# Kernel tuning notes

Measured on AMD Instinct MI355X. Metric: run time of the kernel, lower is better.

The kernel has to match this reference:

```python
import jax, jax.numpy as jnp
import numpy as np

H = 8          # num heads
D = 16         # head dim
HID = 128      # hidden_dim = H * D
NM, ND, NA = 100000, 20000, 50000
E = 300000     # edges per relation
NUM_CLASSES = 8


def setup_inputs() -> dict:
    key = jax.random.key(0)
    ks = jax.random.split(key, 24)
    s = 0.05
    eye = jnp.eye(D, dtype=jnp.float32)
    inp = {
        'x_movie': jax.random.normal(ks[0], (NM, 256), jnp.float32),
        'x_director': jax.random.normal(ks[1], (ND, 128), jnp.float32),
        'x_actor': jax.random.normal(ks[2], (NA, 128), jnp.float32),
        # edge lists per relation: (director->movie, actor->movie, movie->director, movie->actor)
        'src_dm': jax.random.randint(ks[3], (E,), 0, ND),
        'dst_dm': jax.random.randint(ks[4], (E,), 0, NM),
        'src_am': jax.random.randint(ks[5], (E,), 0, NA),
        'dst_am': jax.random.randint(ks[6], (E,), 0, NM),
        'src_md': jax.random.randint(ks[7], (E,), 0, NM),
        'dst_md': jax.random.randint(ks[8], (E,), 0, ND),
        'src_ma': jax.random.randint(ks[9], (E,), 0, NM),
        'dst_ma': jax.random.randint(ks[10], (E,), 0, NA),
        # per-type pre-encoder (use_pre_encoder=True)
        'Wpre_m': jax.random.normal(ks[11], (256, HID), jnp.float32) * s,
        'Wpre_d': jax.random.normal(ks[12], (128, HID), jnp.float32) * s,
        'Wpre_a': jax.random.normal(ks[13], (128, HID), jnp.float32) * s,
        'bpre': jnp.zeros((3, HID), jnp.float32),
        # per-type K/Q/V projections, stacked over the 3 node types
        'Wk': jax.random.normal(ks[14], (3, HID, HID), jnp.float32) * s,
        'bk': jnp.zeros((3, HID), jnp.float32),
        'Wq': jax.random.normal(ks[15], (3, HID, HID), jnp.float32) * s,
        'bq': jnp.zeros((3, HID), jnp.float32),
        'Wv': jax.random.normal(ks[16], (3, HID, HID), jnp.float32) * s,
        'bv': jnp.zeros((3, HID), jnp.float32),
        # per-relation attention / message matrices and priors (4 relations)
        'a_rel': eye + jax.random.normal(ks[17], (4, H, D, D), jnp.float32) * s,
        'm_rel': eye + jax.random.normal(ks[18], (4, H, D, D), jnp.float32) * s,
        'p_rel': jnp.ones((4, H), jnp.float32),
        # per-type skip gate and output projection
        'skip': jnp.ones((3,), jnp.float32),
        'Wa': jax.random.normal(ks[19], (3, HID, HID), jnp.float32) * s,
        'ba': jnp.zeros((3, HID), jnp.float32),
        # final classification head on target node type ('movie')
        'Wlin': jax.random.normal(ks[20], (HID, NUM_CLASSES), jnp.float32) * s,
        'blin': jnp.zeros((NUM_CLASSES,), jnp.float32),
    }
    return inp


def _seg_softmax_agg(alpha, msg, dst, n):
    # softmax over incoming edges of each destination node, then weighted sum of msgs
    m = jax.ops.segment_max(alpha, dst, num_segments=n)      # [n, H]
    m = jnp.where(jnp.isfinite(m), m, 0.0)
    a = jnp.exp(alpha - m[dst])                              # [E, H]
    denom = jax.ops.segment_sum(a, dst, num_segments=n)      # [n, H]
    num = jax.ops.segment_sum(a[:, :, None] * msg, dst, num_segments=n)  # [n, H, D]
    return num / jnp.maximum(denom, 1e-16)[:, :, None]


def reference(x_movie, x_director, x_actor,
              src_dm, dst_dm, src_am, dst_am, src_md, dst_md, src_ma, dst_ma,
              Wpre_m, Wpre_d, Wpre_a, bpre, Wk, bk, Wq, bq, Wv, bv,
              a_rel, m_rel, p_rel, skip, Wa, ba, Wlin, blin):
    # type order: 0=movie, 1=director, 2=actor
    xs = [x_movie @ Wpre_m + bpre[0],
          x_director @ Wpre_d + bpre[1],
          x_actor @ Wpre_a + bpre[2]]
    k = [(x @ Wk[t] + bk[t]).reshape(-1, H, D) for t, x in enumerate(xs)]
    q = [(x @ Wq[t] + bq[t]).reshape(-1, H, D) for t, x in enumerate(xs)]
    v = [(x @ Wv[t] + bv[t]).reshape(-1, H, D) for t, x in enumerate(xs)]

    # (src_type, dst_type, src_idx, dst_idx) per relation
    rels = [(1, 0, src_dm, dst_dm), (2, 0, src_am, dst_am),
            (0, 1, src_md, dst_md), (0, 2, src_ma, dst_ma)]
    scale = 1.0 / np.sqrt(D).astype(np.float32)
    buckets = {0: [], 1: [], 2: []}
    for r, (st, dt, src, dst) in enumerate(rels):
        ke = jnp.einsum('ehd,hdf->ehf', k[st][src], a_rel[r])          # [E,H,D]
        al = jnp.einsum('ehf,ehf->eh', q[dt][dst], ke) * p_rel[r] * scale
        me = jnp.einsum('ehd,hdf->ehf', v[st][src], m_rel[r])          # [E,H,D]
        buckets[dt].append((al, me, dst))

    n = [x.shape[0] for x in xs]
    outs = []
    for t in range(3):
        al = jnp.concatenate([b[0] for b in buckets[t]], axis=0)
        me = jnp.concatenate([b[1] for b in buckets[t]], axis=0)
        dst = jnp.concatenate([b[2] for b in buckets[t]], axis=0)
        agg = _seg_softmax_agg(al, me, dst, n[t]).reshape(n[t], HID)
        h = jax.nn.gelu(agg, approximate=False) @ Wa[t] + ba[t]
        g = jax.nn.sigmoid(skip[t])
        outs.append(g * h + (1.0 - g) * xs[t])

    return outs[0] @ Wlin + blin
```

## Files before the change

### kernel.cpp

```cpp
#include <hip/hip_runtime.h>
#include <hip/hip_bf16.h>
#include <math.h>

#define NM 100000
#define ND 20000
#define NA 50000
#define EDG 300000
#define CAP 32

typedef __attribute__((ext_vector_type(8))) short shortx8;
typedef __attribute__((ext_vector_type(4))) float floatx4;
typedef __attribute__((ext_vector_type(4))) int intx4;

__device__ __forceinline__ float bf2f(unsigned int u) {
    return __uint_as_float(u << 16);
}
__device__ __forceinline__ unsigned short f2bf(float f) {
    unsigned int x = __float_as_uint(f);
    unsigned int r = x + 0x7fffu + ((x >> 16) & 1u);
    return (unsigned short)(r >> 16);
}
__device__ __forceinline__ unsigned short f2bf_fast(float f) {
    return (unsigned short)((__float_as_uint(f) + 0x8000u) >> 16);
}
__device__ __forceinline__ unsigned int pkbf2(float a, float b) {
    return __builtin_amdgcn_perm(__float_as_uint(b) + 0x8000u,
                                 __float_as_uint(a) + 0x8000u,
                                 0x07060302u);
}
__device__ __forceinline__ float gelu_exact(float x) {
    return 0.5f * x * (1.0f + erff(x * 0.70710678118654752f));
}

static const size_t OFF_BT_Q      = 0;
static const size_t OFF_BT_KAMV_D = 73728;
static const size_t OFF_BT_KAMV_A = 139264;
static const size_t OFF_WKA_D     = 204800;
static const size_t OFF_WVM_D     = 270336;
static const size_t OFF_WKA_A     = 335872;
static const size_t OFF_WVM_A     = 401408;
static const size_t OFF_BQ        = 466944;
static const size_t OFF_B_KAMV_D  = 467520;
static const size_t OFF_B_KAMV_A  = 468544;
static const size_t OFF_BKA_D     = 469568;
static const size_t OFF_BVM_D     = 470080;
static const size_t OFF_BKA_A     = 470592;
static const size_t OFF_BVM_A     = 471104;
static const size_t OFF_WALS      = 471616;
static const size_t OFF_BFIN      = 475712;
static const size_t OFF_Q0        = 524288;
static const size_t OFF_SKIPB     = 26124288;
static const size_t OFF_KAMV_D    = 29324288;
static const size_t OFF_KAMV_A    = 39564288;
static const size_t OFF_COUNTS    = 65164288;
static const size_t OFF_SLOTS     = 65564288;
#define KAMV_A_DELTA 10240000

__global__ __launch_bounds__(256) void precompA(
    const float* __restrict__ Wk, const float* __restrict__ bk,
    const float* __restrict__ Wv, const float* __restrict__ bv,
    const float* __restrict__ Wa, const float* __restrict__ ba,
    const float* __restrict__ Wlin, const float* __restrict__ blin,
    const float* __restrict__ a_rel, const float* __restrict__ m_rel,
    const float* __restrict__ p_rel, const float* __restrict__ skip,
    const float* __restrict__ bpre,
    char* __restrict__ ws)
{
    int tid = blockIdx.x * 256 + threadIdx.x;
    if (tid < 65536) {
        int mat = tid >> 14, rem = tid & 16383;
        int e = rem >> 7, hf = rem & 127, h = hf >> 4, f = hf & 15;
        const float* Wsrc; const float* R; float sc; float* dst;
        if (mat == 0)      { Wsrc = Wk + 16384; R = a_rel;        sc = p_rel[h]     * 0.25f; dst = (float*)(ws + OFF_WKA_D); }
        else if (mat == 1) { Wsrc = Wv + 16384; R = m_rel;        sc = 1.0f;                 dst = (float*)(ws + OFF_WVM_D); }
        else if (mat == 2) { Wsrc = Wk + 32768; R = a_rel + 2048; sc = p_rel[8 + h] * 0.25f; dst = (float*)(ws + OFF_WKA_A); }
        else               { Wsrc = Wv + 32768; R = m_rel + 2048; sc = 1.0f;                 dst = (float*)(ws + OFF_WVM_A); }
        float s = 0.0f;
        for (int d = 0; d < 16; d++)
            s += Wsrc[e * 128 + h * 16 + d] * R[h * 256 + d * 16 + f];
        dst[e * 128 + hf] = s * sc;
    } else if (tid < 66048) {
        int idx = tid - 65536;
        int mat = idx >> 7, hf = idx & 127, h = hf >> 4, f = hf & 15;
        const float* bsrc; const float* R; float sc; float* dst;
        if (mat == 0)      { bsrc = bk + 128; R = a_rel;        sc = p_rel[h]     * 0.25f; dst = (float*)(ws + OFF_BKA_D); }
        else if (mat == 1) { bsrc = bv + 128; R = m_rel;        sc = 1.0f;                 dst = (float*)(ws + OFF_BVM_D); }
        else if (mat == 2) { bsrc = bk + 256; R = a_rel + 2048; sc = p_rel[8 + h] * 0.25f; dst = (float*)(ws + OFF_BKA_A); }
        else               { bsrc = bv + 256; R = m_rel + 2048; sc = 1.0f;                 dst = (float*)(ws + OFF_BVM_A); }
        float s = 0.0f;
        for (int d = 0; d < 16; d++)
            s += bsrc[h * 16 + d] * R[h * 256 + d * 16 + f];
        dst[hf] = s * sc;
    } else if (tid < 67072) {
        int idx = tid - 66048;
        int j = idx >> 3, c = idx & 7;
        float g = 1.0f / (1.0f + __expf(-skip[0]));
        float s = 0.0f;
        for (int o = 0; o < 128; o++)
            s += Wa[j * 128 + o] * Wlin[o * 8 + c];
        ((float*)(ws + OFF_WALS))[j * 8 + c] = g * s;
    } else if (tid < 67080) {
        int c = tid - 67072;
        float g = 1.0f / (1.0f + __expf(-skip[0]));
        float s1 = 0.0f, s2 = 0.0f;
        for (int o = 0; o < 128; o++) {
            s1 += ba[o]   * Wlin[o * 8 + c];
            s2 += bpre[o] * Wlin[o * 8 + c];
        }
        ((float*)(ws + OFF_BFIN))[c] = g * s1 + (1.0f - g) * s2 + blin[c];
    } else if (tid < 67080 + NM) {
        ((int*)(ws + OFF_COUNTS))[tid - 67080] = 0;
    }
}

__global__ __launch_bounds__(256) void precompB(
    const float* __restrict__ Wpre_m, const float* __restrict__ Wpre_d,
    const float* __restrict__ Wpre_a, const float* __restrict__ bpre,
    const float* __restrict__ Wq, const float* __restrict__ bq,
    const float* __restrict__ Wlin, const float* __restrict__ skip,
    char* __restrict__ ws)
{
    int tid = blockIdx.x * 256 + threadIdx.x;
    const float* WKA_D = (const float*)(ws + OFF_WKA_D);
    const float* WVM_D = (const float*)(ws + OFF_WVM_D);
    const float* WKA_A = (const float*)(ws + OFF_WKA_A);
    const float* WVM_A = (const float*)(ws + OFF_WVM_A);

    if (tid < 36864) {
        int n = tid >> 8, c = tid & 255;
        float s = 0.0f;
        if (n < 128) {
            for (int e = 0; e < 128; e++)
                s += Wpre_m[c * 128 + e] * Wq[e * 128 + n];
        } else if (n < 136) {
            int cc = n - 128;
            float g = 1.0f / (1.0f + __expf(-skip[0]));
            for (int e = 0; e < 128; e++)
                s += Wpre_m[c * 128 + e] * Wlin[e * 8 + cc];
            s *= (1.0f - g);
        }
        ((unsigned short*)(ws + OFF_BT_Q))[n * 256 + c] = f2bf(s);
    } else if (tid < 69632) {
        int idx = tid - 36864;
        int nrow = idx >> 7, c = idx & 127;
        const float* Wf = (nrow < 128) ? WKA_D : WVM_D;
        int nc = nrow & 127;
        float s = 0.0f;
        for (int e = 0; e < 128; e++)
            s += Wpre_d[c * 128 + e] * Wf[e * 128 + nc];
        ((unsigned short*)(ws + OFF_BT_KAMV_D))[nrow * 128 + c] = f2bf(s);
    } else if (tid < 102400) {
        int idx = tid - 69632;
        int nrow = idx >> 7, c = idx & 127;
        const float* Wf = (nrow < 128) ? WKA_A : WVM_A;
        int nc = nrow & 127;
        float s = 0.0f;
        for (int e = 0; e < 128; e++)
            s += Wpre_a[c * 128 + e] * Wf[e * 128 + nc];
        ((unsigned short*)(ws + OFF_BT_KAMV_A))[nrow * 128 + c] = f2bf(s);
    } else if (tid < 102544) {
        int n = tid - 102400;
        float s = 0.0f;
        if (n < 128) {
            for (int e = 0; e < 128; e++)
                s += bpre[e] * Wq[e * 128 + n];
            s += bq[n];
        }
        ((float*)(ws + OFF_BQ))[n] = s;
    } else if (tid < 102800) {
        int nrow = tid - 102544;
        const float* Wf  = (nrow < 128) ? WKA_D : WVM_D;
        const float* bf_ = (nrow < 128) ? (const float*)(ws + OFF_BKA_D) : (const float*)(ws + OFF_BVM_D);
        int nc = nrow & 127;
        float s = 0.0f;
        for (int e = 0; e < 128; e++)
            s += bpre[128 + e] * Wf[e * 128 + nc];
        ((float*)(ws + OFF_B_KAMV_D))[nrow] = s + bf_[nc];
    } else if (tid < 103056) {
        int nrow = tid - 102800;
        const float* Wf  = (nrow < 128) ? WKA_A : WVM_A;
        const float* bf_ = (nrow < 128) ? (const float*)(ws + OFF_BKA_A) : (const float*)(ws + OFF_BVM_A);
        int nc = nrow & 127;
        float s = 0.0f;
        for (int e = 0; e < 128; e++)
            s += bpre[256 + e] * Wf[e * 128 + nc];
        ((float*)(ws + OFF_B_KAMV_A))[nrow] = s + bf_[nc];
    }
}

__global__ __launch_bounds__(256) void edge_scatter(
    const int* __restrict__ src_dm, const int* __restrict__ dst_dm,
    const int* __restrict__ src_am, const int* __restrict__ dst_am,
    int* __restrict__ counts, int* __restrict__ slots)
{
    int t = blockIdx.x * 256 + threadIdx.x;
    if (t >= 2 * EDG) return;
    int src, dst, delta;
    if (t < EDG) { src = src_dm[t];       dst = dst_dm[t];       delta = 0; }
    else         { src = src_am[t - EDG]; dst = dst_am[t - EDG]; delta = KAMV_A_DELTA; }
    int pos = atomicAdd(&counts[dst], 1);
    if (pos < CAP) slots[(size_t)dst * CAP + pos] = src * 512 + delta;
}

#define MFMA16(a, b, c) __builtin_amdgcn_mfma_f32_16x16x32_bf16(a, b, c, 0, 0, 0)

template<int NT, bool SKIP>
__global__ __launch_bounds__(256, 2) void gemm_m(
    const float* __restrict__ A, int M,
    const unsigned short* __restrict__ BT,
    const float* __restrict__ bias,
    unsigned short* __restrict__ outb, int ldout,
    float* __restrict__ skipb)
{
    __shared__ unsigned short a_lds[128 * 136];
    __shared__ unsigned short b_lds[NT * 16 * 136];
    int tid = threadIdx.x;
    int w = tid >> 6, lane = tid & 63;
    int quad = lane >> 4, low = lane & 15;
    int rbase = blockIdx.x * 128 + w * 32;

    floatx4 acc[2][NT] = {};

    for (int hfi = 0; hfi < 2; hfi++) {
        if (hfi) __syncthreads();
        for (int idx = tid; idx < NT * 16 * 16; idx += 256) {
            int n = idx >> 4, ch = idx & 15;
            *(intx4*)(&b_lds[n * 136 + ch * 8]) =
                *(const intx4*)(&BT[(size_t)n * 256 + hfi * 128 + ch * 8]);
        }
        for (int f = tid; f < 4096; f += 256) {
            int r = f >> 5, c4 = f & 31;
            int rg = blockIdx.x * 128 + r;
            if (rg >= M) rg = M - 1;
            floatx4 v = *(const floatx4*)(A + (size_t)rg * 256 + hfi * 128 + c4 * 4);
            unsigned long long d =
                ((unsigned long long)pkbf2(v[2], v[3]) << 32) | pkbf2(v[0], v[1]);
            *(unsigned long long*)(&a_lds[r * 136 + c4 * 4]) = d;
        }
        __syncthreads();

        #pragma unroll
        for (int ks = 0; ks < 4; ks++) {
            int ko = ks * 32 + quad * 8;
            shortx8 a0 = *(const shortx8*)(&a_lds[(w * 32 + low) * 136 + ko]);
            shortx8 a1 = *(const shortx8*)(&a_lds[(w * 32 + 16 + low) * 136 + ko]);
            #pragma unroll
            for (int nt = 0; nt < NT; nt++) {
                shortx8 b = *(const shortx8*)(&b_lds[(nt * 16 + low) * 136 + ko]);
                acc[0][nt] = MFMA16(a0, b, acc[0][nt]);
                acc[1][nt] = MFMA16(a1, b, acc[1][nt]);
            }
        }
    }

    #pragma unroll
    for (int mt = 0; mt < 2; mt++) {
        #pragma unroll
        for (int nt = 0; nt < NT; nt++) {
            #pragma unroll
            for (int r = 0; r < 4; r++) {
                int row = rbase + mt * 16 + quad * 4 + r;
                if (row >= M) continue;
                int col = nt * 16 + low;
                float v = acc[mt][nt][r] + bias[col];
                if (SKIP && nt == 8) {
                    if (low < 8) skipb[(size_t)row * 8 + low] = v;
                } else {
                    outb[(size_t)row * ldout + col] = f2bf_fast(v);
                }
            }
        }
    }
}

__global__ __launch_bounds__(256, 2) void gemm_kamv(
    const float* __restrict__ A_d, const float* __restrict__ A_a,
    const unsigned short* __restrict__ BT_d, const unsigned short* __restrict__ BT_a,
    const float* __restrict__ bias_d, const float* __restrict__ bias_a,
    unsigned short* __restrict__ out_d, unsigned short* __restrict__ out_a)
{
    __shared__ unsigned short a_lds[128 * 136];
    __shared__ unsigned short b_lds[128 * 136];
    const int NBLK_D = (ND + 127) / 128;
    bool isD = (int)blockIdx.x < NBLK_D;
    const float* A           = isD ? A_d    : A_a;
    const unsigned short* BT = (isD ? BT_d : BT_a) + (size_t)blockIdx.y * 128 * 128;
    const float* bias        = (isD ? bias_d : bias_a) + blockIdx.y * 128;
    unsigned short* outb     = isD ? out_d  : out_a;
    int M  = isD ? ND : NA;
    int bx = isD ? (int)blockIdx.x : (int)blockIdx.x - NBLK_D;
    int col_off = blockIdx.y * 128;

    int tid = threadIdx.x;
    int w = tid >> 6, lane = tid & 63;
    int quad = lane >> 4, low = lane & 15;
    int rbase = bx * 128 + w * 32;

    for (int idx = tid; idx < 2048; idx += 256) {
        int n = idx >> 4, ch = idx & 15;
        *(intx4*)(&b_lds[n * 136 + ch * 8]) =
            *(const intx4*)(&BT[(size_t)n * 128 + ch * 8]);
    }
    for (int f = tid; f < 4096; f += 256) {
        int r = f >> 5, c4 = f & 31;
        int rg = bx * 128 + r;
        if (rg >= M) rg = M - 1;
        floatx4 v = *(const floatx4*)(A + (size_t)rg * 128 + c4 * 4);
        unsigned long long d =
            ((unsigned long long)pkbf2(v[2], v[3]) << 32) | pkbf2(v[0], v[1]);
        *(unsigned long long*)(&a_lds[r * 136 + c4 * 4]) = d;
    }
    __syncthreads();

    floatx4 acc[2][8] = {};
    #pragma unroll
    for (int ks = 0; ks < 4; ks++) {
        int ko = ks * 32 + quad * 8;
        shortx8 a0 = *(const shortx8*)(&a_lds[(w * 32 + low) * 136 + ko]);
        shortx8 a1 = *(const shortx8*)(&a_lds[(w * 32 + 16 + low) * 136 + ko]);
        #pragma unroll
        for (int nt = 0; nt < 8; nt++) {
            shortx8 b = *(const shortx8*)(&b_lds[(nt * 16 + low) * 136 + ko]);
            acc[0][nt] = MFMA16(a0, b, acc[0][nt]);
            acc[1][nt] = MFMA16(a1, b, acc[1][nt]);
        }
    }

    #pragma unroll
    for (int mt = 0; mt < 2; mt++) {
        #pragma unroll
        for (int nt = 0; nt < 8; nt++) {
            #pragma unroll
            for (int r = 0; r < 4; r++) {
                int row = rbase + mt * 16 + quad * 4 + r;
                if (row >= M) continue;
                int col = nt * 16 + low;
                outb[(size_t)row * 256 + col_off + col] = f2bf_fast(acc[mt][nt][r] + bias[col]);
            }
        }
    }
}

__global__ __launch_bounds__(256) void agg_kernel(
    const unsigned short* __restrict__ q0,
    const char* __restrict__ kamv0,
    const int* __restrict__ counts, const int* __restrict__ slots,
    const float* __restrict__ skipb,
    const float* __restrict__ WaLs, const float* __restrict__ bfin,
    float* __restrict__ out)
{
    __shared__ float wals[1032];
    for (int i = threadIdx.x; i < 1024; i += 256) {
        int c = i >> 7, rem = i & 127, j = rem >> 4, L = rem & 15;
        wals[i] = WaLs[(L * 8 + j) * 8 + c];
    }
    if (threadIdx.x < 8) wals[1024 + threadIdx.x] = bfin[threadIdx.x];
    __syncthreads();

    int lane = threadIdx.x & 63;
    int grp = lane >> 4;
    int L   = lane & 15;
    int n = blockIdx.x * 16 + (threadIdx.x >> 6) * 4 + grp;

    intx4 qv = *(const intx4*)(q0 + (size_t)n * 128 + L * 8);
    float qf[8];
    #pragma unroll
    for (int d = 0; d < 4; d++) {
        unsigned int u = (unsigned int)qv[d];
        qf[2 * d]     = __uint_as_float(u << 16);
        qf[2 * d + 1] = __uint_as_float(u & 0xffff0000u);
    }

    int cnt = counts[n];
    cnt = cnt < 0 ? 0 : (cnt > CAP ? CAP : cnt);
    int s0 = slots[(size_t)n * CAP + L];

    float acc[8] = {0, 0, 0, 0, 0, 0, 0, 0};
    float den = 0.0f;
    for (int i = 0; i < cnt; i++) {
        int off = __shfl(s0, (lane & 48) + (i & 15));
        if (__builtin_expect(i >= 16, 0)) off = slots[(size_t)n * CAP + i];
        const char* p = kamv0 + off;
        intx4 ku = *(const intx4*)(p + L * 16);
        intx4 mu = *(const intx4*)(p + 256 + L * 16);
        float ph = 0.0f;
        #pragma unroll
        for (int d = 0; d < 4; d++) {
            unsigned int u = (unsigned int)ku[d];
            ph += qf[2 * d]     * __uint_as_float(u << 16);
            ph += qf[2 * d + 1] * __uint_as_float(u & 0xffff0000u);
        }
        float pf = ph + __shfl_xor(ph, 1);
        float wgt = __expf(fminf(pf, 60.0f));
        den += wgt;
        #pragma unroll
        for (int d = 0; d < 4; d++) {
            unsigned int u = (unsigned int)mu[d];
            acc[2 * d]     += wgt * __uint_as_float(u << 16);
            acc[2 * d + 1] += wgt * __uint_as_float(u & 0xffff0000u);
        }
    }
    float inv = 1.0f / fmaxf(den, 1e-16f);

    float part[8] = {0, 0, 0, 0, 0, 0, 0, 0};
    #pragma unroll
    for (int j = 0; j < 8; j++) {
        float u = gelu_exact(acc[j] * inv);
        #pragma unroll
        for (int c = 0; c < 8; c++)
            part[c] += u * wals[c * 128 + j * 16 + L];
    }

    bool b0 = lane & 1, b1 = lane & 2, b2 = lane & 4;
    float t1[4], t2[2], t3;
    #pragma unroll
    for (int k = 0; k < 4; k++) {
        float send = b0 ? part[k] : part[4 + k];
        float got  = __shfl_xor(send, 1);
        t1[k] = (b0 ? part[4 + k] : part[k]) + got;
    }
    #pragma unroll
    for (int k = 0; k < 2; k++) {
        float send = b1 ? t1[k] : t1[2 + k];
        float got  = __shfl_xor(send, 2);
        t2[k] = (b1 ? t1[2 + k] : t1[k]) + got;
    }
    {
        float send = b2 ? t2[0] : t2[1];
        float got  = __shfl_xor(send, 4);
        t3 = (b2 ? t2[1] : t2[0]) + got;
    }
    t3 += __shfl_xor(t3, 8);
    if (L < 8) {
        int c = 4 * (L & 1) + 2 * ((L >> 1) & 1) + ((L >> 2) & 1);
        out[(size_t)n * 8 + c] = t3 + skipb[(size_t)n * 8 + c] + wals[1024 + c];
    }
}

extern "C" void kernel_launch(void* const* d_in, const int* in_sizes, int n_in,
                              void* d_out, int out_size, void* d_ws, size_t ws_size,
                              hipStream_t stream) {
    (void)in_sizes; (void)n_in; (void)out_size; (void)ws_size;
    const float* x_movie    = (const float*)d_in[0];
    const float* x_director = (const float*)d_in[1];
    const float* x_actor    = (const float*)d_in[2];
    const int* src_dm = (const int*)d_in[3];
    const int* dst_dm = (const int*)d_in[4];
    const int* src_am = (const int*)d_in[5];
    const int* dst_am = (const int*)d_in[6];
    const float* Wpre_m = (const float*)d_in[11];
    const float* Wpre_d = (const float*)d_in[12];
    const float* Wpre_a = (const float*)d_in[13];
    const float* bpre   = (const float*)d_in[14];
    const float* Wk     = (const float*)d_in[15];
    const float* bk     = (const float*)d_in[16];
    const float* Wq     = (const float*)d_in[17];
    const float* bq     = (const float*)d_in[18];
    const float* Wv     = (const float*)d_in[19];
    const float* bv     = (const float*)d_in[20];
    const float* a_rel  = (const float*)d_in[21];
    const float* m_rel  = (const float*)d_in[22];
    const float* p_rel  = (const float*)d_in[23];
    const float* skip   = (const float*)d_in[24];
    const float* Wa     = (const float*)d_in[25];
    const float* ba     = (const float*)d_in[26];
    const float* Wlin   = (const float*)d_in[27];
    const float* blin   = (const float*)d_in[28];

    char* ws = (char*)d_ws;
    float* out = (float*)d_out;

    precompA<<<(67080 + NM + 255) / 256, 256, 0, stream>>>(
        Wk, bk, Wv, bv, Wa, ba, Wlin, blin,
        a_rel, m_rel, p_rel, skip, bpre, ws);
    precompB<<<403, 256, 0, stream>>>(Wpre_m, Wpre_d, Wpre_a, bpre,
                                      Wq, bq, Wlin, skip, ws);

    edge_scatter<<<(2 * EDG + 255) / 256, 256, 0, stream>>>(
        src_dm, dst_dm, src_am, dst_am,
        (int*)(ws + OFF_COUNTS), (int*)(ws + OFF_SLOTS));

    gemm_m<9, true><<<(NM + 127) / 128, 256, 0, stream>>>(
        x_movie, NM, (const unsigned short*)(ws + OFF_BT_Q),
        (const float*)(ws + OFF_BQ),
        (unsigned short*)(ws + OFF_Q0), 128, (float*)(ws + OFF_SKIPB));

    gemm_kamv<<<dim3((ND + 127) / 128 + (NA + 127) / 128, 2), 256, 0, stream>>>(
        x_director, x_actor,
        (const unsigned short*)(ws + OFF_BT_KAMV_D),
        (const unsigned short*)(ws + OFF_BT_KAMV_A),
        (const float*)(ws + OFF_B_KAMV_D), (const float*)(ws + OFF_B_KAMV_A),
        (unsigned short*)(ws + OFF_KAMV_D), (unsigned short*)(ws + OFF_KAMV_A));

    agg_kernel<<<NM / 16, 256, 0, stream>>>(
        (const unsigned short*)(ws + OFF_Q0),
        (const char*)(ws + OFF_KAMV_D),
        (const int*)(ws + OFF_COUNTS), (const int*)(ws + OFF_SLOTS),
        (const float*)(ws + OFF_SKIPB),
        (const float*)(ws + OFF_WALS), (const float*)(ws + OFF_BFIN), out);
}
```

Measured before the change: 446.9 us.

## Merge precompute, edge scatter and GEMM launches; transpose weights for vectorized dot products

The precompB and edge_scatter kernels are folded into one launch, and the movie and director/actor GEMMs into a single gemm_all launch with block-range dispatch. This cuts launch count and the idle tails between dependent small kernels. Wq and the fused K/V weights are stored transposed so the precompute dot products read contiguous memory with float4 loads instead of strided loops. The GEMM loads are restructured to fetch global data into registers before writing to LDS. WQT reuses the SKIPB workspace offset, which is only safe because the transposed Wq is consumed before gemm_all writes skipb.

```diff
diff --git a/kernel.cpp b/kernel.cpp
--- a/kernel.cpp
+++ b/kernel.cpp
@@ -7,6 +7,7 @@
 #define NA 50000
 #define EDG 300000
 #define CAP 32
+#define NBLK_M 782
 
 typedef __attribute__((ext_vector_type(8))) short shortx8;
 typedef __attribute__((ext_vector_type(4))) float floatx4;
@@ -50,6 +51,7 @@
 static const size_t OFF_BFIN      = 475712;
 static const size_t OFF_Q0        = 524288;
 static const size_t OFF_SKIPB     = 26124288;
+static const size_t OFF_WQT       = 26124288;
 static const size_t OFF_KAMV_D    = 29324288;
 static const size_t OFF_KAMV_A    = 39564288;
 static const size_t OFF_COUNTS    = 65164288;
@@ -63,7 +65,7 @@
     const float* __restrict__ Wlin, const float* __restrict__ blin,
     const float* __restrict__ a_rel, const float* __restrict__ m_rel,
     const float* __restrict__ p_rel, const float* __restrict__ skip,
-    const float* __restrict__ bpre,
+    const float* __restrict__ bpre, const float* __restrict__ Wq,
     char* __restrict__ ws)
 {
     int tid = blockIdx.x * 256 + threadIdx.x;
@@ -78,7 +80,7 @@
         float s = 0.0f;
         for (int d = 0; d < 16; d++)
             s += Wsrc[e * 128 + h * 16 + d] * R[h * 256 + d * 16 + f];
-        dst[e * 128 + hf] = s * sc;
+        dst[hf * 128 + e] = s * sc;
     } else if (tid < 66048) {
         int idx = tid - 65536;
         int mat = idx >> 7, hf = idx & 127, h = hf >> 4, f = hf & 15;
@@ -108,30 +110,61 @@
             s2 += bpre[o] * Wlin[o * 8 + c];
         }
         ((float*)(ws + OFF_BFIN))[c] = g * s1 + (1.0f - g) * s2 + blin[c];
-    } else if (tid < 67080 + NM) {
-        ((int*)(ws + OFF_COUNTS))[tid - 67080] = 0;
-    }
-}
-
-__global__ __launch_bounds__(256) void precompB(
+    } else if (tid < 83464) {
+        int i = tid - 67080;
+        int n = i >> 7, e = i & 127;
+        ((float*)(ws + OFF_WQT))[n * 128 + e] = Wq[e * 128 + n];
+    } else if (tid < 83464 + NM) {
+        ((int*)(ws + OFF_COUNTS))[tid - 83464] = 0;
+    }
+}
+
+__device__ __forceinline__ float dot128(const float* __restrict__ a,
+                                        const float* __restrict__ b) {
+    const floatx4* x = (const floatx4*)a;
+    const floatx4* y = (const floatx4*)b;
+    float s = 0.0f;
+    #pragma unroll
+    for (int i = 0; i < 32; i++) {
+        floatx4 u = x[i], v = y[i];
+        s += u[0] * v[0] + u[1] * v[1] + u[2] * v[2] + u[3] * v[3];
+    }
+    return s;
+}
+
+__global__ __launch_bounds__(256) void prep_scat(
+    const int* __restrict__ src_dm, const int* __restrict__ dst_dm,
+    const int* __restrict__ src_am, const int* __restrict__ dst_am,
     const float* __restrict__ Wpre_m, const float* __restrict__ Wpre_d,
     const float* __restrict__ Wpre_a, const float* __restrict__ bpre,
-    const float* __restrict__ Wq, const float* __restrict__ bq,
-    const float* __restrict__ Wlin, const float* __restrict__ skip,
+    const float* __restrict__ bq, const float* __restrict__ Wlin,
+    const float* __restrict__ skip,
     char* __restrict__ ws)
 {
-    int tid = blockIdx.x * 256 + threadIdx.x;
+    if (blockIdx.x < 2344) {
+        int t = blockIdx.x * 256 + threadIdx.x;
+        if (t >= 2 * EDG) return;
+        int src, dst, delta;
+        if (t < EDG) { src = src_dm[t];       dst = dst_dm[t];       delta = 0; }
+        else         { src = src_am[t - EDG]; dst = dst_am[t - EDG]; delta = KAMV_A_DELTA; }
+        int* counts = (int*)(ws + OFF_COUNTS);
+        int* slots  = (int*)(ws + OFF_SLOTS);
+        int pos = atomicAdd(&counts[dst], 1);
+        if (pos < CAP) slots[(size_t)dst * CAP + pos] = src * 512 + delta;
+        return;
+    }
+    int tid = (blockIdx.x - 2344) * 256 + threadIdx.x;
     const float* WKA_D = (const float*)(ws + OFF_WKA_D);
     const float* WVM_D = (const float*)(ws + OFF_WVM_D);
     const float* WKA_A = (const float*)(ws + OFF_WKA_A);
     const float* WVM_A = (const float*)(ws + OFF_WVM_A);
+    const float* WqT   = (const float*)(ws + OFF_WQT);
 
     if (tid < 36864) {
         int n = tid >> 8, c = tid & 255;
         float s = 0.0f;
         if (n < 128) {
-            for (int e = 0; e < 128; e++)
-                s += Wpre_m[c * 128 + e] * Wq[e * 128 + n];
+            s = dot128(Wpre_m + c * 128, WqT + n * 128);
         } else if (n < 136) {
             int cc = n - 128;
             float g = 1.0f / (1.0f + __expf(-skip[0]));
@@ -143,199 +176,184 @@
     } else if (tid < 69632) {
         int idx = tid - 36864;
         int nrow = idx >> 7, c = idx & 127;
-        const float* Wf = (nrow < 128) ? WKA_D : WVM_D;
+        const float* WfT = (nrow < 128) ? WKA_D : WVM_D;
         int nc = nrow & 127;
-        float s = 0.0f;
-        for (int e = 0; e < 128; e++)
-            s += Wpre_d[c * 128 + e] * Wf[e * 128 + nc];
+        float s = dot128(Wpre_d + c * 128, WfT + nc * 128);
         ((unsigned short*)(ws + OFF_BT_KAMV_D))[nrow * 128 + c] = f2bf(s);
     } else if (tid < 102400) {
         int idx = tid - 69632;
         int nrow = idx >> 7, c = idx & 127;
-        const float* Wf = (nrow < 128) ? WKA_A : WVM_A;
+        const float* WfT = (nrow < 128) ? WKA_A : WVM_A;
         int nc = nrow & 127;
-        float s = 0.0f;
-        for (int e = 0; e < 128; e++)
-            s += Wpre_a[c * 128 + e] * Wf[e * 128 + nc];
+        float s = dot128(Wpre_a + c * 128, WfT + nc * 128);
         ((unsigned short*)(ws + OFF_BT_KAMV_A))[nrow * 128 + c] = f2bf(s);
     } else if (tid < 102544) {
         int n = tid - 102400;
         float s = 0.0f;
-        if (n < 128) {
-            for (int e = 0; e < 128; e++)
-                s += bpre[e] * Wq[e * 128 + n];
-            s += bq[n];
-        }
+        if (n < 128) s = dot128(bpre, WqT + n * 128) + bq[n];
         ((float*)(ws + OFF_BQ))[n] = s;
     } else if (tid < 102800) {
         int nrow = tid - 102544;
-        const float* Wf  = (nrow < 128) ? WKA_D : WVM_D;
+        const float* WfT = (nrow < 128) ? WKA_D : WVM_D;
         const float* bf_ = (nrow < 128) ? (const float*)(ws + OFF_BKA_D) : (const float*)(ws + OFF_BVM_D);
         int nc = nrow & 127;
-        float s = 0.0f;
-        for (int e = 0; e < 128; e++)
-            s += bpre[128 + e] * Wf[e * 128 + nc];
-        ((float*)(ws + OFF_B_KAMV_D))[nrow] = s + bf_[nc];
+        ((float*)(ws + OFF_B_KAMV_D))[nrow] = dot128(bpre + 128, WfT + nc * 128) + bf_[nc];
     } else if (tid < 103056) {
         int nrow = tid - 102800;
-        const float* Wf  = (nrow < 128) ? WKA_A : WVM_A;
+        const float* WfT = (nrow < 128) ? WKA_A : WVM_A;
         const float* bf_ = (nrow < 128) ? (const float*)(ws + OFF_BKA_A) : (const float*)(ws + OFF_BVM_A);
         int nc = nrow & 127;
-        float s = 0.0f;
-        for (int e = 0; e < 128; e++)
-            s += bpre[256 + e] * Wf[e * 128 + nc];
-        ((float*)(ws + OFF_B_KAMV_A))[nrow] = s + bf_[nc];
-    }
-}
-
-__global__ __launch_bounds__(256) void edge_scatter(
-    const int* __restrict__ src_dm, const int* __restrict__ dst_dm,
-    const int* __restrict__ src_am, const int* __restrict__ dst_am,
-    int* __restrict__ counts, int* __restrict__ slots)
-{
-    int t = blockIdx.x * 256 + threadIdx.x;
-    if (t >= 2 * EDG) return;
-    int src, dst, delta;
-    if (t < EDG) { src = src_dm[t];       dst = dst_dm[t];       delta = 0; }
-    else         { src = src_am[t - EDG]; dst = dst_am[t - EDG]; delta = KAMV_A_DELTA; }
-    int pos = atomicAdd(&counts[dst], 1);
-    if (pos < CAP) slots[(size_t)dst * CAP + pos] = src * 512 + delta;
+        ((float*)(ws + OFF_B_KAMV_A))[nrow] = dot128(bpre + 256, WfT + nc * 128) + bf_[nc];
+    }
 }
 
 #define MFMA16(a, b, c) __builtin_amdgcn_mfma_f32_16x16x32_bf16(a, b, c, 0, 0, 0)
 
-template<int NT, bool SKIP>
-__global__ __launch_bounds__(256, 2) void gemm_m(
-    const float* __restrict__ A, int M,
-    const unsigned short* __restrict__ BT,
-    const float* __restrict__ bias,
-    unsigned short* __restrict__ outb, int ldout,
-    float* __restrict__ skipb)
+__global__ __launch_bounds__(256, 2) void gemm_all(
+    const float* __restrict__ xm, const float* __restrict__ xd,
+    const float* __restrict__ xa,
+    const unsigned short* __restrict__ btq,
+    const unsigned short* __restrict__ btd,
+    const unsigned short* __restrict__ bta,
+    const float* __restrict__ bq,
+    const float* __restrict__ bbd, const float* __restrict__ bba,
+    unsigned short* __restrict__ q0, float* __restrict__ skipb,
+    unsigned short* __restrict__ outd, unsigned short* __restrict__ outa)
 {
     __shared__ unsigned short a_lds[128 * 136];
-    __shared__ unsigned short b_lds[NT * 16 * 136];
+    __shared__ unsigned short b_lds[144 * 136];
     int tid = threadIdx.x;
     int w = tid >> 6, lane = tid & 63;
     int quad = lane >> 4, low = lane & 15;
-    int rbase = blockIdx.x * 128 + w * 32;
-
-    floatx4 acc[2][NT] = {};
-
-    for (int hfi = 0; hfi < 2; hfi++) {
-        if (hfi) __syncthreads();
-        for (int idx = tid; idx < NT * 16 * 16; idx += 256) {
-            int n = idx >> 4, ch = idx & 15;
-            *(intx4*)(&b_lds[n * 136 + ch * 8]) =
-                *(const intx4*)(&BT[(size_t)n * 256 + hfi * 128 + ch * 8]);
-        }
-        for (int f = tid; f < 4096; f += 256) {
-            int r = f >> 5, c4 = f & 31;
-            int rg = blockIdx.x * 128 + r;
-            if (rg >= M) rg = M - 1;
-            floatx4 v = *(const floatx4*)(A + (size_t)rg * 256 + hfi * 128 + c4 * 4);
+    int bx = blockIdx.x;
+
+    if (bx < NBLK_M) {
+        int row0 = bx * 128;
+        floatx4 acc[2][9] = {};
+        for (int hfi = 0; hfi < 2; hfi++) {
+            if (hfi) __syncthreads();
+            intx4 bvv[9];
+            #pragma unroll
+            for (int it = 0; it < 9; it++) {
+                int idx = it * 256 + tid, n = idx >> 4, ch = idx & 15;
+                bvv[it] = *(const intx4*)&btq[(size_t)n * 256 + hfi * 128 + ch * 8];
+            }
+            floatx4 av[16];
+            #pragma unroll
+            for (int it = 0; it < 16; it++) {
+                int f = it * 256 + tid, r = f >> 5, c4 = f & 31;
+                int rg = row0 + r; if (rg >= NM) rg = NM - 1;
+                av[it] = *(const floatx4*)(xm + (size_t)rg * 256 + hfi * 128 + c4 * 4);
+            }
+            #pragma unroll
+            for (int it = 0; it < 9; it++) {
+                int idx = it * 256 + tid, n = idx >> 4, ch = idx & 15;
+                *(intx4*)&b_lds[n * 136 + ch * 8] = bvv[it];
+            }
+            #pragma unroll
+            for (int it = 0; it < 16; it++) {
+                int f = it * 256 + tid, r = f >> 5, c4 = f & 31;
+                unsigned long long d =
+                    ((unsigned long long)pkbf2(av[it][2], av[it][3]) << 32) |
+                    pkbf2(av[it][0], av[it][1]);
+                *(unsigned long long*)&a_lds[r * 136 + c4 * 4] = d;
+            }
+            __syncthreads();
+            #pragma unroll
+            for (int ks = 0; ks < 4; ks++) {
+                int ko = ks * 32 + quad * 8;
+                shortx8 a0 = *(const shortx8*)&a_lds[(w * 32 + low) * 136 + ko];
+                shortx8 a1 = *(const shortx8*)&a_lds[(w * 32 + 16 + low) * 136 + ko];
+                #pragma unroll
+                for (int nt = 0; nt < 9; nt++) {
+                    shortx8 b = *(const shortx8*)&b_lds[(nt * 16 + low) * 136 + ko];
+                    acc[0][nt] = MFMA16(a0, b, acc[0][nt]);
+                    acc[1][nt] = MFMA16(a1, b, acc[1][nt]);
+                }
+            }
+        }
+        int rb = row0 + w * 32;
+        #pragma unroll
+        for (int mt = 0; mt < 2; mt++) {
+            #pragma unroll
+            for (int nt = 0; nt < 9; nt++) {
+                #pragma unroll
+                for (int r = 0; r < 4; r++) {
+                    int row = rb + mt * 16 + quad * 4 + r;
+                    if (row >= NM) continue;
+                    int col = nt * 16 + low;
+                    float v = acc[mt][nt][r] + bq[col];
+                    if (nt == 8) {
+                        if (low < 8) skipb[(size_t)row * 8 + low] = v;
+                    } else {
+                        q0[(size_t)row * 128 + col] = f2bf_fast(v);
+                    }
+                }
+            }
+        }
+    } else {
+        int rem = bx - NBLK_M;
+        const float* A; const unsigned short* BT; const float* bias;
+        unsigned short* outb; int M, kbx, cofs;
+        if (rem < 157)      { A = xd; BT = btd;             bias = bbd;       outb = outd; M = ND; kbx = rem;       cofs = 0;   }
+        else if (rem < 314) { A = xd; BT = btd + 128 * 128; bias = bbd + 128; outb = outd; M = ND; kbx = rem - 157; cofs = 128; }
+        else if (rem < 705) { A = xa; BT = bta;             bias = bba;       outb = outa; M = NA; kbx = rem - 314; cofs = 0;   }
+        else                { A = xa; BT = bta + 128 * 128; bias = bba + 128; outb = outa; M = NA; kbx = rem - 705; cofs = 128; }
+        int row0 = kbx * 128;
+
+        intx4 bvv[8];
+        #pragma unroll
+        for (int it = 0; it < 8; it++) {
+            int idx = it * 256 + tid, n = idx >> 4, ch = idx & 15;
+            bvv[it] = *(const intx4*)&BT[(size_t)n * 128 + ch * 8];
+        }
+        floatx4 av[16];
+        #pragma unroll
+        for (int it = 0; it < 16; it++) {
+            int f = it * 256 + tid, r = f >> 5, c4 = f & 31;
+            int rg = row0 + r; if (rg >= M) rg = M - 1;
+            av[it] = *(const floatx4*)(A + (size_t)rg * 128 + c4 * 4);
+        }
+        #pragma unroll
+        for (int it = 0; it < 8; it++) {
+            int idx = it * 256 + tid, n = idx >> 4, ch = idx & 15;
+            *(intx4*)&b_lds[n * 136 + ch * 8] = bvv[it];
+        }
+        #pragma unroll
+        for (int it = 0; it < 16; it++) {
+            int f = it * 256 + tid, r = f >> 5, c4 = f & 31;
             unsigned long long d =
-                ((unsigned long long)pkbf2(v[2], v[3]) << 32) | pkbf2(v[0], v[1]);
-            *(unsigned long long*)(&a_lds[r * 136 + c4 * 4]) = d;
+                ((unsigned long long)pkbf2(av[it][2], av[it][3]) << 32) |
+                pkbf2(av[it][0], av[it][1]);
+            *(unsigned long long*)&a_lds[r * 136 + c4 * 4] = d;
         }
         __syncthreads();
 
+        floatx4 acc[2][8] = {};
         #pragma unroll
         for (int ks = 0; ks < 4; ks++) {
             int ko = ks * 32 + quad * 8;
-            shortx8 a0 = *(const shortx8*)(&a_lds[(w * 32 + low) * 136 + ko]);
-            shortx8 a1 = *(const shortx8*)(&a_lds[(w * 32 + 16 + low) * 136 + ko]);
-            #pragma unroll
-            for (int nt = 0; nt < NT; nt++) {
-                shortx8 b = *(const shortx8*)(&b_lds[(nt * 16 + low) * 136 + ko]);
+            shortx8 a0 = *(const shortx8*)&a_lds[(w * 32 + low) * 136 + ko];
+            shortx8 a1 = *(const shortx8*)&a_lds[(w * 32 + 16 + low) * 136 + ko];
+            #pragma unroll
+            for (int nt = 0; nt < 8; nt++) {
+                shortx8 b = *(const shortx8*)&b_lds[(nt * 16 + low) * 136 + ko];
                 acc[0][nt] = MFMA16(a0, b, acc[0][nt]);
                 acc[1][nt] = MFMA16(a1, b, acc[1][nt]);
             }
         }
-    }
-
-    #pragma unroll
-    for (int mt = 0; mt < 2; mt++) {
-        #pragma unroll
-        for (int nt = 0; nt < NT; nt++) {
-            #pragma unroll
-            for (int r = 0; r < 4; r++) {
-                int row = rbase + mt * 16 + quad * 4 + r;
-                if (row >= M) continue;
-                int col = nt * 16 + low;
-                float v = acc[mt][nt][r] + bias[col];
-                if (SKIP && nt == 8) {
-                    if (low < 8) skipb[(size_t)row * 8 + low] = v;
-                } else {
-                    outb[(size_t)row * ldout + col] = f2bf_fast(v);
+        int rb = row0 + w * 32;
+        #pragma unroll
+        for (int mt = 0; mt < 2; mt++) {
+            #pragma unroll
+            for (int nt = 0; nt < 8; nt++) {
+                #pragma unroll
+                for (int r = 0; r < 4; r++) {
+                    int row = rb + mt * 16 + quad * 4 + r;
+                    if (row >= M) continue;
+                    int col = nt * 16 + low;
+                    outb[(size_t)row * 256 + cofs + col] = f2bf_fast(acc[mt][nt][r] + bias[col]);
                 }
-            }
-        }
-    }
-}
-
-__global__ __launch_bounds__(256, 2) void gemm_kamv(
-    const float* __restrict__ A_d, const float* __restrict__ A_a,
-    const unsigned short* __restrict__ BT_d, const unsigned short* __restrict__ BT_a,
-    const float* __restrict__ bias_d, const float* __restrict__ bias_a,
-    unsigned short* __restrict__ out_d, unsigned short* __restrict__ out_a)
-{
-    __shared__ unsigned short a_lds[128 * 136];
-    __shared__ unsigned short b_lds[128 * 136];
-    const int NBLK_D = (ND + 127) / 128;
-    bool isD = (int)blockIdx.x < NBLK_D;
-    const float* A           = isD ? A_d    : A_a;
-    const unsigned short* BT = (isD ? BT_d : BT_a) + (size_t)blockIdx.y * 128 * 128;
-    const float* bias        = (isD ? bias_d : bias_a) + blockIdx.y * 128;
-    unsigned short* outb     = isD ? out_d  : out_a;
-    int M  = isD ? ND : NA;
-    int bx = isD ? (int)blockIdx.x : (int)blockIdx.x - NBLK_D;
-    int col_off = blockIdx.y * 128;
-
-    int tid = threadIdx.x;
-    int w = tid >> 6, lane = tid & 63;
-    int quad = lane >> 4, low = lane & 15;
-    int rbase = bx * 128 + w * 32;
-
-    for (int idx = tid; idx < 2048; idx += 256) {
-        int n = idx >> 4, ch = idx & 15;
-        *(intx4*)(&b_lds[n * 136 + ch * 8]) =
-            *(const intx4*)(&BT[(size_t)n * 128 + ch * 8]);
-    }
-    for (int f = tid; f < 4096; f += 256) {
-        int r = f >> 5, c4 = f & 31;
-        int rg = bx * 128 + r;
-        if (rg >= M) rg = M - 1;
-        floatx4 v = *(const floatx4*)(A + (size_t)rg * 128 + c4 * 4);
-        unsigned long long d =
-            ((unsigned long long)pkbf2(v[2], v[3]) << 32) | pkbf2(v[0], v[1]);
-        *(unsigned long long*)(&a_lds[r * 136 + c4 * 4]) = d;
-    }
-    __syncthreads();
-
-    floatx4 acc[2][8] = {};
-    #pragma unroll
-    for (int ks = 0; ks < 4; ks++) {
-        int ko = ks * 32 + quad * 8;
-        shortx8 a0 = *(const shortx8*)(&a_lds[(w * 32 + low) * 136 + ko]);
-        shortx8 a1 = *(const shortx8*)(&a_lds[(w * 32 + 16 + low) * 136 + ko]);
-        #pragma unroll
-        for (int nt = 0; nt < 8; nt++) {
-            shortx8 b = *(const shortx8*)(&b_lds[(nt * 16 + low) * 136 + ko]);
-            acc[0][nt] = MFMA16(a0, b, acc[0][nt]);
-            acc[1][nt] = MFMA16(a1, b, acc[1][nt]);
-        }
-    }
-
-    #pragma unroll
-    for (int mt = 0; mt < 2; mt++) {
-        #pragma unroll
-        for (int nt = 0; nt < 8; nt++) {
-            #pragma unroll
-            for (int r = 0; r < 4; r++) {
-                int row = rbase + mt * 16 + quad * 4 + r;
-                if (row >= M) continue;
-                int col = nt * 16 + low;
-                outb[(size_t)row * 256 + col_off + col] = f2bf_fast(acc[mt][nt][r] + bias[col]);
             }
         }
     }
@@ -470,26 +488,22 @@
     char* ws = (char*)d_ws;
     float* out = (float*)d_out;
 
-    precompA<<<(67080 + NM + 255) / 256, 256, 0, stream>>>(
+    precompA<<<(83464 + NM + 255) / 256, 256, 0, stream>>>(
         Wk, bk, Wv, bv, Wa, ba, Wlin, blin,
-        a_rel, m_rel, p_rel, skip, bpre, ws);
-    precompB<<<403, 256, 0, stream>>>(Wpre_m, Wpre_d, Wpre_a, bpre,
-                                      Wq, bq, Wlin, skip, ws);
-
-    edge_scatter<<<(2 * EDG + 255) / 256, 256, 0, stream>>>(
+        a_rel, m_rel, p_rel, skip, bpre, Wq, ws);
+
+    prep_scat<<<2344 + 403, 256, 0, stream>>>(
         src_dm, dst_dm, src_am, dst_am,
-        (int*)(ws + OFF_COUNTS), (int*)(ws + OFF_SLOTS));
-
-    gemm_m<9, true><<<(NM + 127) / 128, 256, 0, stream>>>(
-        x_movie, NM, (const unsigned short*)(ws + OFF_BT_Q),
-        (const float*)(ws + OFF_BQ),
-        (unsigned short*)(ws + OFF_Q0), 128, (float*)(ws + OFF_SKIPB));
-
-    gemm_kamv<<<dim3((ND + 127) / 128 + (NA + 127) / 128, 2), 256, 0, stream>>>(
-        x_director, x_actor,
+        Wpre_m, Wpre_d, Wpre_a, bpre, bq, Wlin, skip, ws);
+
+    gemm_all<<<NBLK_M + 1096, 256, 0, stream>>>(
+        x_movie, x_director, x_actor,
+        (const unsigned short*)(ws + OFF_BT_Q),
         (const unsigned short*)(ws + OFF_BT_KAMV_D),
         (const unsigned short*)(ws + OFF_BT_KAMV_A),
+        (const float*)(ws + OFF_BQ),
         (const float*)(ws + OFF_B_KAMV_D), (const float*)(ws + OFF_B_KAMV_A),
+        (unsigned short*)(ws + OFF_Q0), (float*)(ws + OFF_SKIPB),
         (unsigned short*)(ws + OFF_KAMV_D), (unsigned short*)(ws + OFF_KAMV_A));
 
     agg_kernel<<<NM / 16, 256, 0, stream>>>(
```

Measured after the change: 398.4 us. 10.9% less time.
